# Performance work log

Hardware: AMD Instinct MI355X
Metric: run time of the kernel (lower is better)

Reference implementation:

```python
import jax, jax.numpy as jnp
import numpy as np

N = 20000   # nodes
R = 8       # base out-degree (ring circulant), plus self-loop
K = 3       # hops: supports of A, A^2, A^3
IN_DIM = 128
HID = 64


def _edges(m):
    # support of A^m for circulant ring with self-loops: dst i receives from (i-t) mod N, t=0..m*R
    deg = m * R + 1
    dst = np.repeat(np.arange(N, dtype=np.int32), deg)
    src = (dst - np.tile(np.arange(deg, dtype=np.int32), N)) % N
    return jnp.asarray(src), jnp.asarray(dst)


def setup_inputs() -> dict:
    key = jax.random.key(0)
    ks = jax.random.split(key, 8)
    def xavier(k, shape):
        fan_out, fan_in = shape[0], shape[1]
        std = np.float32(np.sqrt(2.0) * np.sqrt(2.0 / (fan_in + fan_out)))  # gain('relu')
        return jax.random.normal(k, shape, jnp.float32) * std
    inp = {
        "h": jax.random.normal(ks[0], (N, IN_DIM), jnp.float32),
        "fc_enc": xavier(ks[1], (HID, IN_DIM)),
        "diff_enc": xavier(ks[2], (HID, IN_DIM)),
        "att_enc": xavier(ks[3], (HID, 1)),
        "fc_dec": xavier(ks[4], (IN_DIM, HID)),
        "diff_dec": xavier(ks[5], (IN_DIM, HID)),
        "att_dec": xavier(ks[6], (IN_DIM, 1)),
        "att_comb": xavier(ks[7], (HID, 1)),
    }
    for m in range(1, K + 1):
        s, d = _edges(m)
        inp[f"src{m}"] = s
        inp[f"dst{m}"] = d
    return inp


def _gdn_layer(src, dst, h, Wfc, Wdiff, att, use_elu):
    z = h @ Wfc.T                      # [N, out]
    hd = h @ Wdiff.T                   # [N, out]
    d = hd[src] - hd[dst]              # edge gather-diff [E, out]
    e = jax.nn.leaky_relu(d @ att)     # [E, 1], torch default slope 0.01
    # edge softmax over incoming edges of each dst node
    emax = jax.ops.segment_max(e, dst, num_segments=N)
    ex = jnp.exp(e - emax[dst])
    den = jax.ops.segment_sum(ex, dst, num_segments=N)
    a = ex / den[dst]                  # [E, 1]
    agg = jax.ops.segment_sum(a * d, dst, num_segments=N)  # scatter-sum
    out = z + agg
    return jax.nn.elu(out) if use_elu else out


def reference(h, fc_enc, diff_enc, att_enc, fc_dec, diff_dec, att_dec, att_comb,
              src1, dst1, src2, dst2, src3, dst3):
    hops = [(src1, dst1), (src2, dst2), (src3, dst3)]
    Zs = [_gdn_layer(s, d, h, fc_enc, diff_enc, att_enc, True) for s, d in hops]
    e = jnp.concatenate([Z @ att_comb for Z in Zs], axis=-1)   # [N, K]
    a = jax.nn.softmax(jax.nn.leaky_relu(e), axis=-1)          # [N, K]
    z = jnp.einsum('nk,nhk->nh', a, jnp.stack(Zs, axis=-1))    # hop-attention combine
    # decoder runs on the last hop's graph (A^K), as in the torch code
    x = _gdn_layer(src3, dst3, z, fc_dec, diff_dec, att_dec, False)
    return x
```

## Files before the change

### kernel.cpp

```cpp
#include <hip/hip_runtime.h>
#include <math.h>

#define NN 20000

typedef __attribute__((ext_vector_type(8))) short short8;
typedef __attribute__((ext_vector_type(4))) float floatx4;

__device__ __forceinline__ int wrapN(int r) {
    if (r < 0) r += NN;
    if (r >= NN) r -= NN;
    return r;
}
__device__ __forceinline__ unsigned f2bf(float f) {
    unsigned int u = __float_as_uint(f);
    u = (u + 0x7FFFu + ((u >> 16) & 1u)) >> 16;
    return u;
}

__global__ __launch_bounds__(256) void k0_prep(
    const float* __restrict__ fce, const float* __restrict__ dfe,
    const float* __restrict__ atte, const float* __restrict__ fcd,
    const float* __restrict__ dfd, const float* __restrict__ attd,
    unsigned short* __restrict__ Wenc, unsigned short* __restrict__ Wdec,
    float* __restrict__ uenc, float* __restrict__ vdec)
{
    const int idx = blockIdx.x * 256 + threadIdx.x;
    {
        int r = idx >> 7, k = idx & 127;
        float v = (r < 64) ? fce[r * 128 + k] : dfe[(r - 64) * 128 + k];
        Wenc[r * 128 + k] = (unsigned short)f2bf(v);
    }
    {
        int r = idx >> 6, k = idx & 63;
        float v = (r < 128) ? fcd[r * 64 + k] : dfd[(r - 128) * 64 + k];
        Wdec[r * 64 + k] = (unsigned short)f2bf(v);
    }
    if (blockIdx.x == 0 && threadIdx.x < 128) {
        int k = threadIdx.x; float s = 0.f;
        for (int j = 0; j < 64; j++) s = fmaf(atte[j], dfe[j * 128 + k], s);
        uenc[k] = s;
    }
    if (blockIdx.x == 1 && threadIdx.x < 64) {
        int k = threadIdx.x; float s = 0.f;
        for (int c = 0; c < 128; c++) s = fmaf(attd[c], dfd[c * 64 + k], s);
        vdec[k] = s;
    }
}

__global__ __launch_bounds__(256) void kA_enc(
    const float* __restrict__ h, const unsigned short* __restrict__ Wenc,
    const float* __restrict__ uenc, const float* __restrict__ attc,
    const float* __restrict__ vdec, unsigned short* __restrict__ zcb,
    float* __restrict__ gd)
{
    __shared__ __align__(16) float smem[3848];
    unsigned short* Hs = (unsigned short*)smem;
    float* hdw = smem;
    float* zw  = smem + 2720;
    float* gw  = smem + 3808;

    const int tid  = threadIdx.x;
    const int n0   = blockIdx.x * 16;
    const int lane = tid & 63;
    const int wv   = tid >> 6;
    const int m16  = lane & 15;
    const int quad = lane >> 4;

    for (int idx = tid; idx < 768; idx += 256) {
        int r = idx >> 4, c = (idx & 15) << 3;
        const float* hp = h + wrapN(n0 - 24 + r) * 128 + c;
        float4 a = *(const float4*)hp;
        float4 b = *(const float4*)(hp + 4);
        uint4 pk;
        pk.x = f2bf(a.x) | (f2bf(a.y) << 16);
        pk.y = f2bf(a.z) | (f2bf(a.w) << 16);
        pk.z = f2bf(b.x) | (f2bf(b.y) << 16);
        pk.w = f2bf(b.z) | (f2bf(b.w) << 16);
        *(uint4*)(Hs + r * 136 + c) = pk;
    }
    for (int idx = tid; idx < 320; idx += 256) {
        int r = idx >> 3, sub = idx & 7;
        const float* hp = h + wrapN(n0 - 24 + r) * 128 + sub * 16;
        const float* up = uenc + sub * 16;
        float s = 0.f;
#pragma unroll
        for (int j = 0; j < 4; j++) {
            float4 hv = *(const float4*)(hp + 4 * j);
            float4 uv = *(const float4*)(up + 4 * j);
            s += hv.x * uv.x + hv.y * uv.y + hv.z * uv.z + hv.w * uv.w;
        }
#pragma unroll
        for (int off = 1; off <= 4; off <<= 1) s += __shfl_xor(s, off, 64);
        if (sub == 0) gw[r] = s;
    }
    __syncthreads();

    floatx4 acc[3][2];
#pragma unroll
    for (int a = 0; a < 3; a++)
#pragma unroll
        for (int b = 0; b < 2; b++) acc[a][b] = (floatx4){0.f, 0.f, 0.f, 0.f};

#pragma unroll
    for (int ks = 0; ks < 4; ks++) {
        const int kk = ks * 32 + quad * 8;
        const int jr0 = 32 * wv + m16;
        short8 B0 = *(const short8*)(Wenc + jr0 * 128 + kk);
        short8 B1 = *(const short8*)(Wenc + (jr0 + 16) * 128 + kk);
        short8 A[3];
#pragma unroll
        for (int mt = 0; mt < 3; mt++)
            A[mt] = *(short8*)(Hs + (mt * 16 + m16) * 136 + kk);
#pragma unroll
        for (int mt = 0; mt < 3; mt++) {
            acc[mt][0] = __builtin_amdgcn_mfma_f32_16x16x32_bf16(A[mt], B0, acc[mt][0], 0, 0, 0);
            acc[mt][1] = __builtin_amdgcn_mfma_f32_16x16x32_bf16(A[mt], B1, acc[mt][1], 0, 0, 0);
        }
    }
    __syncthreads();

#pragma unroll
    for (int mt = 0; mt < 3; mt++)
#pragma unroll
        for (int nt2 = 0; nt2 < 2; nt2++)
#pragma unroll
            for (int r = 0; r < 4; r++) {
                const int row = mt * 16 + quad * 4 + r;
                const int col = 32 * wv + nt2 * 16 + m16;
                const float val = acc[mt][nt2][r];
                if (col >= 64) { if (row < 40) hdw[row * 68 + (col - 64)] = val; }
                else if (row >= 24 && row < 40) zw[(row - 24) * 68 + col] = val;
            }
    __syncthreads();

    const int wvid = tid >> 6;
    const int half = (tid >> 5) & 1;
    const int l    = tid & 31;
    const float2 ac = *(const float2*)(attc + 2 * l);
    const float2 vd = *(const float2*)(vdec + 2 * l);

    for (int it = 0; it < 2; it++) {
        const int li   = 8 * it + 2 * wvid + half;
        const int node = n0 + li;
        const int loc  = 24 + li;

        const float g0 = gw[loc];
        const int t = l;
        float d = 0.f;
        if (t >= 1 && t < 25) {
            d = gw[loc - t] - g0;
            d = d > 0.f ? d : 0.01f * d;
        }
        float dm = (t < 25) ? d : -1e30f;
#pragma unroll
        for (int off = 16; off; off >>= 1) dm = fmaxf(dm, __shfl_xor(dm, off, 64));
        const float e = (t < 25) ? __expf(d - dm) : 0.f;
        float s1 = (t < 9) ? e : 0.f, s2 = (t < 17) ? e : 0.f, s3 = e;
#pragma unroll
        for (int off = 16; off; off >>= 1) {
            s1 += __shfl_xor(s1, off, 64);
            s2 += __shfl_xor(s2, off, 64);
            s3 += __shfl_xor(s3, off, 64);
        }
        const float rd0 = 1.f / s1, rd1 = 1.f / s2, rd2 = 1.f / s3;

        const float2 zi = *(const float2*)(zw + li * 68 + 2 * l);
        const float2 h0 = *(const float2*)(hdw + loc * 68 + 2 * l);

        float2 s = {0.f, 0.f};
        float2 Z[3]; float eh[3];
#pragma unroll
        for (int m = 0; m < 3; m++) {
            const int lo = (m == 0) ? 0 : (m == 1 ? 9 : 17);
            const int hi = (m == 0) ? 9 : (m == 1 ? 17 : 25);
#pragma unroll
            for (int t2 = lo; t2 < hi; t2++) {
                const float et = __shfl(e, (half << 5) + t2, 64);
                const float2 hv = *(const float2*)(hdw + (loc - t2) * 68 + 2 * l);
                s.x = fmaf(et, hv.x, s.x);
                s.y = fmaf(et, hv.y, s.y);
            }
            const float rden = (m == 0) ? rd0 : (m == 1 ? rd1 : rd2);
            float ox = zi.x + s.x * rden - h0.x;
            float oy = zi.y + s.y * rden - h0.y;
            Z[m].x = ox > 0.f ? ox : __expf(ox) - 1.f;
            Z[m].y = oy > 0.f ? oy : __expf(oy) - 1.f;
            float p = Z[m].x * ac.x + Z[m].y * ac.y;
#pragma unroll
            for (int off = 16; off; off >>= 1) p += __shfl_xor(p, off, 64);
            eh[m] = p;
        }
#pragma unroll
        for (int m = 0; m < 3; m++) eh[m] = eh[m] > 0.f ? eh[m] : 0.01f * eh[m];
        const float mx = fmaxf(eh[0], fmaxf(eh[1], eh[2]));
        const float w0 = __expf(eh[0] - mx), w1 = __expf(eh[1] - mx), w2 = __expf(eh[2] - mx);
        const float wd = 1.f / (w0 + w1 + w2);
        float2 o;
        o.x = (w0 * Z[0].x + w1 * Z[1].x + w2 * Z[2].x) * wd;
        o.y = (w0 * Z[0].y + w1 * Z[1].y + w2 * Z[2].y) * wd;
        *(unsigned int*)(zcb + node * 64 + 2 * l) =
            f2bf(o.x) | (f2bf(o.y) << 16);
        float q = o.x * vd.x + o.y * vd.y;
#pragma unroll
        for (int off = 16; off; off >>= 1) q += __shfl_xor(q, off, 64);
        if (l == 0) gd[node] = q;
    }
}

__global__ __launch_bounds__(256) void kB_dec(
    const unsigned short* __restrict__ zcb, const unsigned short* __restrict__ Wdec,
    const float* __restrict__ gd, float* __restrict__ out)
{
    __shared__ __align__(16) float smem[7928];
    unsigned short* Zs  = (unsigned short*)smem;
    unsigned short* hdB = (unsigned short*)smem;
    float* zdw = smem + 2304;
    float* h0w = smem + 4480;
    unsigned short* Eb = (unsigned short*)(smem + 6656);
    float* gw  = smem + 7808;
    float* dmw = smem + 7864;
    float* rdw = smem + 7896;

    const int tid  = threadIdx.x;
    const int tile = blockIdx.x >> 1;
    const int ch   = blockIdx.x & 1;
    const int n0   = tile * 32;
    const int lane = tid & 63;
    const int wv   = tid >> 6;
    const int m16  = lane & 15;
    const int quad = lane >> 4;

    if (tid < 56) gw[tid] = gd[wrapN(n0 - 24 + tid)];

    for (int idx = tid; idx < 512; idx += 256) {
        int r = idx >> 3, c = (idx & 7) << 3;
        *(short8*)(Zs + r * 72 + c) =
            *(const short8*)(zcb + wrapN(n0 - 24 + r) * 64 + c);
    }
    __syncthreads();

    floatx4 acc[4][2];
#pragma unroll
    for (int a = 0; a < 4; a++)
#pragma unroll
        for (int b = 0; b < 2; b++) acc[a][b] = (floatx4){0.f, 0.f, 0.f, 0.f};

#pragma unroll
    for (int ks = 0; ks < 2; ks++) {
        const int kk = ks * 32 + quad * 8;
        const int c0 = 32 * wv + m16;
        const int wr0 = (c0 < 64) ? (ch * 64 + c0) : (128 + ch * 64 + (c0 - 64));
        const int c1 = c0 + 16;
        const int wr1 = (c1 < 64) ? (ch * 64 + c1) : (128 + ch * 64 + (c1 - 64));
        short8 B0 = *(const short8*)(Wdec + wr0 * 64 + kk);
        short8 B1 = *(const short8*)(Wdec + wr1 * 64 + kk);
        short8 A[4];
#pragma unroll
        for (int mt = 0; mt < 4; mt++)
            A[mt] = *(short8*)(Zs + (mt * 16 + m16) * 72 + kk);
#pragma unroll
        for (int mt = 0; mt < 4; mt++) {
            acc[mt][0] = __builtin_amdgcn_mfma_f32_16x16x32_bf16(A[mt], B0, acc[mt][0], 0, 0, 0);
            acc[mt][1] = __builtin_amdgcn_mfma_f32_16x16x32_bf16(A[mt], B1, acc[mt][1], 0, 0, 0);
        }
    }
    __syncthreads();

#pragma unroll
    for (int mt = 0; mt < 4; mt++)
#pragma unroll
        for (int nt2 = 0; nt2 < 2; nt2++) {
            const int colL = 32 * wv + nt2 * 16 + m16;
            const int rowB = mt * 16 + quad * 4;
            if (colL >= 64) {
                const int f = colL - 64;
                if (rowB < 56) {
                    uint2 pk;
                    pk.x = f2bf(acc[mt][nt2][0]) | (f2bf(acc[mt][nt2][1]) << 16);
                    pk.y = f2bf(acc[mt][nt2][2]) | (f2bf(acc[mt][nt2][3]) << 16);
                    *(uint2*)(hdB + f * 72 + rowB) = pk;
                }
#pragma unroll
                for (int r = 0; r < 4; r++) {
                    const int row = rowB + r;
                    if (row >= 24 && row < 56) h0w[(row - 24) * 68 + f] = acc[mt][nt2][r];
                }
            } else {
#pragma unroll
                for (int r = 0; r < 4; r++) {
                    const int row = rowB + r;
                    if (row >= 24 && row < 56) zdw[(row - 24) * 68 + colL] = acc[mt][nt2][r];
                }
            }
        }
    for (int idx = tid; idx < 512; idx += 256) {
        int f = idx >> 3, kk = 56 + ((idx & 7) << 1);
        *(unsigned*)(hdB + f * 72 + kk) = 0;
    }
    __syncthreads();

    if (tid < 32) {
        const float g0 = gw[tid + 24];
        float em = 0.f;
        for (int t = 1; t < 25; t++) {
            float d = gw[tid + 24 - t] - g0;
            d = d > 0.f ? d : 0.01f * d;
            em = fmaxf(em, d);
        }
        float den = __expf(-em);
        for (int t = 1; t < 25; t++) {
            float d = gw[tid + 24 - t] - g0;
            d = d > 0.f ? d : 0.01f * d;
            den += __expf(d - em);
        }
        dmw[tid] = em;
        rdw[tid] = 1.f / den;
    }
    __syncthreads();

    for (int idx = tid; idx < 1152; idx += 256) {
        const int n  = idx / 36;
        const int kk = (idx - n * 36) * 2;
        const float g0 = gw[n + 24];
        const float em = dmw[n], rd = rdw[n];
        unsigned pk = 0;
#pragma unroll
        for (int j = 0; j < 2; j++) {
            const int k = kk + j;
            const bool in = (k >= n) && (k <= n + 24);
            const int kc = in ? k : 0;
            float d = gw[kc] - g0;
            d = d > 0.f ? d : 0.01f * d;
            const float e = in ? __expf(d - em) * rd : 0.f;
            pk |= f2bf(e) << (16 * j);
        }
        *(unsigned*)(Eb + n * 72 + kk) = pk;
    }
    __syncthreads();

    floatx4 wacc[2];
    wacc[0] = (floatx4){0.f, 0.f, 0.f, 0.f};
    wacc[1] = (floatx4){0.f, 0.f, 0.f, 0.f};
#pragma unroll
    for (int ks = 0; ks < 2; ks++) {
        const int kk = ks * 32 + quad * 8;
        short8 Bf = *(short8*)(hdB + (wv * 16 + m16) * 72 + kk);
        short8 A0 = *(short8*)(Eb + m16 * 72 + kk);
        short8 A1 = *(short8*)(Eb + (16 + m16) * 72 + kk);
        wacc[0] = __builtin_amdgcn_mfma_f32_16x16x32_bf16(A0, Bf, wacc[0], 0, 0, 0);
        wacc[1] = __builtin_amdgcn_mfma_f32_16x16x32_bf16(A1, Bf, wacc[1], 0, 0, 0);
    }

#pragma unroll
    for (int mt2 = 0; mt2 < 2; mt2++)
#pragma unroll
        for (int r = 0; r < 4; r++) {
            const int n = mt2 * 16 + quad * 4 + r;
            const int f = wv * 16 + m16;
            const float o = zdw[n * 68 + f] + wacc[mt2][r] - h0w[n * 68 + f];
            out[(n0 + n) * 128 + ch * 64 + f] = o;
        }
}

extern "C" void kernel_launch(void* const* d_in, const int* in_sizes, int n_in,
                              void* d_out, int out_size, void* d_ws, size_t ws_size,
                              hipStream_t stream)
{
    const float* h        = (const float*)d_in[0];
    const float* fc_enc   = (const float*)d_in[1];
    const float* diff_enc = (const float*)d_in[2];
    const float* att_enc  = (const float*)d_in[3];
    const float* fc_dec   = (const float*)d_in[4];
    const float* diff_dec = (const float*)d_in[5];
    const float* att_dec  = (const float*)d_in[6];
    const float* att_comb = (const float*)d_in[7];

    float* out = (float*)d_out;
    float* ws  = (float*)d_ws;
    float*          uenc = ws;
    float*          vdec = ws + 128;
    float*          gd   = ws + 192;
    unsigned short* zcb  = (unsigned short*)(ws + 192 + NN);
    unsigned short* Wenc = zcb + NN * 64;
    unsigned short* Wdec = Wenc + 128 * 128;
    (void)ws_size; (void)in_sizes; (void)n_in; (void)out_size;

    hipLaunchKernelGGL(k0_prep, dim3(64), dim3(256), 0, stream,
                       fc_enc, diff_enc, att_enc, fc_dec, diff_dec, att_dec,
                       Wenc, Wdec, uenc, vdec);
    hipLaunchKernelGGL(kA_enc, dim3(NN / 16), dim3(256), 0, stream,
                       h, Wenc, uenc, att_comb, vdec, zcb, gd);
    hipLaunchKernelGGL(kB_dec, dim3(2 * (NN / 32)), dim3(256), 0, stream,
                       zcb, Wdec, gd, out);
}
```

Before: 123.2 us.

## Compute encoder edge-softmax aggregation with MFMA over banded attention matrix

Replaces the per-thread scalar FMA loop over up to 25 neighbours in the encoder kernel with a bf16 MFMA product of a banded attention-weight matrix (Eb, one row per hop/node) and a transposed bf16 copy of the diff projection. Softmax statistics go to shared memory first, then the normalized weights are built and fed to MFMA, and the hop-attention combine and decoder-gate dot products are reduced across waves through shared partial sums. The aim is to cut VALU and LDS traffic in the aggregation step. In exchange it adds more shared memory, several extra block barriers, and bf16 rounding of the attention weights and hd values.

Result: no change. 124.2 us (+0.8%).

```diff
diff --git a/kernel.cpp b/kernel.cpp
--- a/kernel.cpp
+++ b/kernel.cpp
@@ -53,11 +53,17 @@
     const float* __restrict__ vdec, unsigned short* __restrict__ zcb,
     float* __restrict__ gd)
 {
-    __shared__ __align__(16) float smem[3848];
-    unsigned short* Hs = (unsigned short*)smem;
-    float* hdw = smem;
-    float* zw  = smem + 2720;
-    float* gw  = smem + 3808;
+    __shared__ __align__(16) float smem[6616];
+    unsigned short* Hs  = (unsigned short*)smem;
+    unsigned short* hdB = (unsigned short*)smem;
+    float* zw   = smem + 2304;
+    float* h0w  = smem + 3392;
+    unsigned short* Eb = (unsigned short*)(smem + 4480);
+    float* gw   = smem + 6208;
+    float* stat = smem + 6248;
+    float* part = smem + 6312;
+    float* prt2 = smem + 6504;
+    float* wfac = smem + 6568;
 
     const int tid  = threadIdx.x;
     const int n0   = blockIdx.x * 16;
@@ -122,89 +128,169 @@
 #pragma unroll
     for (int mt = 0; mt < 3; mt++)
 #pragma unroll
-        for (int nt2 = 0; nt2 < 2; nt2++)
-#pragma unroll
-            for (int r = 0; r < 4; r++) {
-                const int row = mt * 16 + quad * 4 + r;
-                const int col = 32 * wv + nt2 * 16 + m16;
-                const float val = acc[mt][nt2][r];
-                if (col >= 64) { if (row < 40) hdw[row * 68 + (col - 64)] = val; }
-                else if (row >= 24 && row < 40) zw[(row - 24) * 68 + col] = val;
+        for (int nt2 = 0; nt2 < 2; nt2++) {
+            const int colL = 32 * wv + nt2 * 16 + m16;
+            const int rowB = mt * 16 + quad * 4;
+            if (colL >= 64) {
+                const int f = colL - 64;
+                if (rowB < 40) {
+                    uint2 pk;
+                    pk.x = f2bf(acc[mt][nt2][0]) | (f2bf(acc[mt][nt2][1]) << 16);
+                    pk.y = f2bf(acc[mt][nt2][2]) | (f2bf(acc[mt][nt2][3]) << 16);
+                    *(uint2*)(hdB + f * 72 + rowB) = pk;
+                }
+#pragma unroll
+                for (int r = 0; r < 4; r++) {
+                    const int row = rowB + r;
+                    if (row >= 24 && row < 40) h0w[(row - 24) * 68 + f] = acc[mt][nt2][r];
+                }
+            } else {
+#pragma unroll
+                for (int r = 0; r < 4; r++) {
+                    const int row = rowB + r;
+                    if (row >= 24 && row < 40) zw[(row - 24) * 68 + colL] = acc[mt][nt2][r];
+                }
             }
-    __syncthreads();
-
-    const int wvid = tid >> 6;
-    const int half = (tid >> 5) & 1;
-    const int l    = tid & 31;
-    const float2 ac = *(const float2*)(attc + 2 * l);
-    const float2 vd = *(const float2*)(vdec + 2 * l);
-
-    for (int it = 0; it < 2; it++) {
-        const int li   = 8 * it + 2 * wvid + half;
-        const int node = n0 + li;
-        const int loc  = 24 + li;
-
-        const float g0 = gw[loc];
-        const int t = l;
-        float d = 0.f;
-        if (t >= 1 && t < 25) {
-            d = gw[loc - t] - g0;
+        }
+    for (int idx = tid; idx < 1024; idx += 256) {
+        int f = idx >> 4, kk = 40 + ((idx & 15) << 1);
+        *(unsigned*)(hdB + f * 72 + kk) = 0;
+    }
+    {
+        const int half = (tid >> 5) & 1;
+        const int l    = tid & 31;
+        for (int it = 0; it < 2; it++) {
+            const int li  = 8 * it + 2 * wv + half;
+            const int loc = 24 + li;
+            const float g0 = gw[loc];
+            const int t = l;
+            float d = 0.f;
+            if (t >= 1 && t < 25) {
+                d = gw[loc - t] - g0;
+                d = d > 0.f ? d : 0.01f * d;
+            }
+            float dm = (t < 25) ? d : -1e30f;
+#pragma unroll
+            for (int off = 16; off; off >>= 1) dm = fmaxf(dm, __shfl_xor(dm, off, 64));
+            const float e = (t < 25) ? __expf(d - dm) : 0.f;
+            float s1 = (t < 9) ? e : 0.f, s2 = (t < 17) ? e : 0.f, s3 = e;
+#pragma unroll
+            for (int off = 16; off; off >>= 1) {
+                s1 += __shfl_xor(s1, off, 64);
+                s2 += __shfl_xor(s2, off, 64);
+                s3 += __shfl_xor(s3, off, 64);
+            }
+            if (l == 0) {
+                stat[li * 4 + 0] = dm;
+                stat[li * 4 + 1] = 1.f / s1;
+                stat[li * 4 + 2] = 1.f / s2;
+                stat[li * 4 + 3] = 1.f / s3;
+            }
+        }
+    }
+    __syncthreads();
+
+    for (int idx = tid; idx < 1728; idx += 256) {
+        const int np = idx / 36;
+        const int kp = (idx - np * 36) * 2;
+        const int m  = np >> 4;
+        const int li = np & 15;
+        const float g0 = gw[li + 24];
+        const float em = stat[li * 4 + 0];
+        const float rd = stat[li * 4 + 1 + m];
+        const int hi = (m == 0) ? 9 : (m == 1 ? 17 : 25);
+        unsigned pk = 0;
+#pragma unroll
+        for (int j = 0; j < 2; j++) {
+            const int k = kp + j;
+            const int t = li + 24 - k;
+            const bool in = (t >= 0) && (t < hi);
+            const int kc = in ? k : (li + 24);
+            float d = gw[kc] - g0;
             d = d > 0.f ? d : 0.01f * d;
-        }
-        float dm = (t < 25) ? d : -1e30f;
-#pragma unroll
-        for (int off = 16; off; off >>= 1) dm = fmaxf(dm, __shfl_xor(dm, off, 64));
-        const float e = (t < 25) ? __expf(d - dm) : 0.f;
-        float s1 = (t < 9) ? e : 0.f, s2 = (t < 17) ? e : 0.f, s3 = e;
-#pragma unroll
-        for (int off = 16; off; off >>= 1) {
-            s1 += __shfl_xor(s1, off, 64);
-            s2 += __shfl_xor(s2, off, 64);
-            s3 += __shfl_xor(s3, off, 64);
-        }
-        const float rd0 = 1.f / s1, rd1 = 1.f / s2, rd2 = 1.f / s3;
-
-        const float2 zi = *(const float2*)(zw + li * 68 + 2 * l);
-        const float2 h0 = *(const float2*)(hdw + loc * 68 + 2 * l);
-
-        float2 s = {0.f, 0.f};
-        float2 Z[3]; float eh[3];
+            const float e = in ? __expf(d - em) * rd : 0.f;
+            pk |= f2bf(e) << (16 * j);
+        }
+        *(unsigned*)(Eb + np * 72 + kp) = pk;
+    }
+    __syncthreads();
+
+    floatx4 wacc[3];
+#pragma unroll
+    for (int a = 0; a < 3; a++) wacc[a] = (floatx4){0.f, 0.f, 0.f, 0.f};
+#pragma unroll
+    for (int ks = 0; ks < 2; ks++) {
+        const int kk = ks * 32 + quad * 8;
+        short8 Bf = *(short8*)(hdB + (wv * 16 + m16) * 72 + kk);
+        short8 A0 = *(short8*)(Eb + m16 * 72 + kk);
+        short8 A1 = *(short8*)(Eb + (16 + m16) * 72 + kk);
+        short8 A2 = *(short8*)(Eb + (32 + m16) * 72 + kk);
+        wacc[0] = __builtin_amdgcn_mfma_f32_16x16x32_bf16(A0, Bf, wacc[0], 0, 0, 0);
+        wacc[1] = __builtin_amdgcn_mfma_f32_16x16x32_bf16(A1, Bf, wacc[1], 0, 0, 0);
+        wacc[2] = __builtin_amdgcn_mfma_f32_16x16x32_bf16(A2, Bf, wacc[2], 0, 0, 0);
+    }
+
+    const int f = wv * 16 + m16;
+    const float ac = attc[f];
+    const float vd = vdec[f];
+    float zh[4], hh[4];
+#pragma unroll
+    for (int r = 0; r < 4; r++) {
+        const int li = quad * 4 + r;
+        zh[r] = zw[li * 68 + f];
+        hh[r] = h0w[li * 68 + f];
+    }
+    float Zr[3][4];
+#pragma unroll
+    for (int mt = 0; mt < 3; mt++)
+#pragma unroll
+        for (int r = 0; r < 4; r++) {
+            const float o = zh[r] + wacc[mt][r] - hh[r];
+            const float Z = o > 0.f ? o : __expf(o) - 1.f;
+            Zr[mt][r] = Z;
+            float p = Z * ac;
+#pragma unroll
+            for (int off = 1; off <= 8; off <<= 1) p += __shfl_xor(p, off, 64);
+            if (m16 == 0) part[(mt * 16 + quad * 4 + r) * 4 + wv] = p;
+        }
+    __syncthreads();
+
+    if (tid < 16) {
+        float eh[3];
 #pragma unroll
         for (int m = 0; m < 3; m++) {
-            const int lo = (m == 0) ? 0 : (m == 1 ? 9 : 17);
-            const int hi = (m == 0) ? 9 : (m == 1 ? 17 : 25);
-#pragma unroll
-            for (int t2 = lo; t2 < hi; t2++) {
-                const float et = __shfl(e, (half << 5) + t2, 64);
-                const float2 hv = *(const float2*)(hdw + (loc - t2) * 68 + 2 * l);
-                s.x = fmaf(et, hv.x, s.x);
-                s.y = fmaf(et, hv.y, s.y);
-            }
-            const float rden = (m == 0) ? rd0 : (m == 1 ? rd1 : rd2);
-            float ox = zi.x + s.x * rden - h0.x;
-            float oy = zi.y + s.y * rden - h0.y;
-            Z[m].x = ox > 0.f ? ox : __expf(ox) - 1.f;
-            Z[m].y = oy > 0.f ? oy : __expf(oy) - 1.f;
-            float p = Z[m].x * ac.x + Z[m].y * ac.y;
-#pragma unroll
-            for (int off = 16; off; off >>= 1) p += __shfl_xor(p, off, 64);
-            eh[m] = p;
-        }
-#pragma unroll
-        for (int m = 0; m < 3; m++) eh[m] = eh[m] > 0.f ? eh[m] : 0.01f * eh[m];
+            float s = part[(m * 16 + tid) * 4 + 0] + part[(m * 16 + tid) * 4 + 1]
+                    + part[(m * 16 + tid) * 4 + 2] + part[(m * 16 + tid) * 4 + 3];
+            eh[m] = s > 0.f ? s : 0.01f * s;
+        }
         const float mx = fmaxf(eh[0], fmaxf(eh[1], eh[2]));
         const float w0 = __expf(eh[0] - mx), w1 = __expf(eh[1] - mx), w2 = __expf(eh[2] - mx);
         const float wd = 1.f / (w0 + w1 + w2);
-        float2 o;
-        o.x = (w0 * Z[0].x + w1 * Z[1].x + w2 * Z[2].x) * wd;
-        o.y = (w0 * Z[0].y + w1 * Z[1].y + w2 * Z[2].y) * wd;
-        *(unsigned int*)(zcb + node * 64 + 2 * l) =
-            f2bf(o.x) | (f2bf(o.y) << 16);
-        float q = o.x * vd.x + o.y * vd.y;
-#pragma unroll
-        for (int off = 16; off; off >>= 1) q += __shfl_xor(q, off, 64);
-        if (l == 0) gd[node] = q;
-    }
+        wfac[0 * 16 + tid] = w0 * wd;
+        wfac[1 * 16 + tid] = w1 * wd;
+        wfac[2 * 16 + tid] = w2 * wd;
+    }
+    __syncthreads();
+
+    float q[4];
+#pragma unroll
+    for (int r = 0; r < 4; r++) {
+        const int li = quad * 4 + r;
+        const float zc = wfac[li] * Zr[0][r] + wfac[16 + li] * Zr[1][r]
+                       + wfac[32 + li] * Zr[2][r];
+        zcb[(n0 + li) * 64 + f] = (unsigned short)f2bf(zc);
+        q[r] = zc * vd;
+    }
+#pragma unroll
+    for (int r = 0; r < 4; r++) {
+#pragma unroll
+        for (int off = 1; off <= 8; off <<= 1) q[r] += __shfl_xor(q[r], off, 64);
+        if (m16 == 0) prt2[(quad * 4 + r) * 4 + wv] = q[r];
+    }
+    __syncthreads();
+    if (tid < 16)
+        gd[n0 + tid] = prt2[tid * 4 + 0] + prt2[tid * 4 + 1]
+                     + prt2[tid * 4 + 2] + prt2[tid * 4 + 3];
 }
 
 __global__ __launch_bounds__(256) void kB_dec(
```
